# Optimization experiments

Hardware: AMD Instinct MI355X
Metric: run time of the kernel (lower is better)

The kernel has to match this reference:

```python
import jax, jax.numpy as jnp
import numpy as np

B, N, D = 8, 2048, 256
C = 8192  # codebook_size
H = 1     # num_codebooks


def setup_inputs() -> dict:
    key = jax.random.key(0)
    k1, k2 = jax.random.split(key)
    x = jax.random.normal(k1, (B, N, D), dtype=jnp.float32)
    # kaiming_uniform_ on [H, C, D]: bound = sqrt(6 / fan_in), fan_in = C*D for a 3D tensor
    bound = float(np.sqrt(6.0 / (C * D)))
    embed = jax.random.uniform(k2, (H, C, D), dtype=jnp.float32, minval=-bound, maxval=bound)
    return {"x": x, "embed": embed}


def reference(x, embed):
    # x: [B, N, D]; module adds a codebook dim since ndim < 4, flattens to [H, B*N, D]
    flat = x.reshape(1, -1, x.shape[-1]).astype(jnp.float32)  # [H, M, D], M = B*N
    # squared euclidean distance (argmin identical to argmin of cdist p=2)
    x2 = jnp.sum(flat * flat, axis=-1, keepdims=True)              # [H, M, 1]
    e2 = jnp.sum(embed * embed, axis=-1)[:, None, :]               # [H, 1, C]
    xe = jnp.einsum('hmd,hcd->hmc', flat, embed)                   # [H, M, C]
    d2 = x2 - 2.0 * xe + e2                                        # [H, M, C]
    # sample_codebook_temp == 0 -> pure argmax of -dist == argmin of dist
    ind = jnp.argmin(d2, axis=-1)                                  # [H, M]
    quantize = jnp.take(embed[0], ind[0], axis=0).reshape(x.shape) # [B, N, D]
    embed_ind = ind.reshape(x.shape[:-1])                          # [B, N]
    return quantize, embed_ind
```

## Files before the change

kernel.cpp:

```cpp
#include <hip/hip_runtime.h>
#include <hip/hip_bf16.h>

#define M_TOT 16384
#define D_DIM 256
#define C_TOT 8192
#define NCH 4
#define CCH (C_TOT / NCH)
#define QOFF (M_TOT * D_DIM)
#define NPART 8

typedef _Float16 f16;
typedef __attribute__((ext_vector_type(8))) _Float16 f16x8;
typedef __attribute__((ext_vector_type(4))) float f32x4;

#define WS_X2 0
#define WS_E2 (M_TOT)
#define WS_BV (M_TOT + C_TOT)
#define WS_BI (WS_BV + NPART * M_TOT)
#define WS_SPL (WS_BI + NPART * M_TOT)
#define XH_OFF ((size_t)0)
#define XL_OFF ((size_t)M_TOT * D_DIM)
#define EH_OFF ((size_t)2 * M_TOT * D_DIM)
#define EL_OFF ((size_t)2 * M_TOT * D_DIM + (size_t)C_TOT * D_DIM)
#define SPL_HALFS ((size_t)2 * M_TOT * D_DIM + (size_t)2 * C_TOT * D_DIM)
#define WS_NEED ((size_t)WS_SPL * 4 + SPL_HALFS * 2)

__device__ __forceinline__ void gll16(const void* g, void* l) {
    __builtin_amdgcn_global_load_lds((const __attribute__((address_space(1))) void*)g,
                                     (__attribute__((address_space(3))) void*)l, 16, 0, 0);
}

__global__ void split_kernel(const float* __restrict__ x, const float* __restrict__ e,
                             f16* __restrict__ sp, float* __restrict__ x2, float* __restrict__ e2)
{
    int row  = blockIdx.x * 4 + (threadIdx.x >> 6);
    int lane = threadIdx.x & 63;
    bool isx = row < M_TOT;
    int r = isx ? row : row - M_TOT;
    const float* src = (isx ? x : e) + (size_t)r * D_DIM;
    float4 v = *(const float4*)(src + lane * 4);
    float s = v.x * v.x + v.y * v.y + v.z * v.z + v.w * v.w;
    #pragma unroll
    for (int off = 32; off >= 1; off >>= 1) s += __shfl_xor(s, off, 64);
    float sc = isx ? 256.0f : 16384.0f;
    float a[4] = {v.x * sc, v.y * sc, v.z * sc, v.w * sc};
    union { f16 h[4]; ushort4 u; } hh, ll;
    #pragma unroll
    for (int i = 0; i < 4; ++i) {
        f16 h = (f16)a[i];
        hh.h[i] = h;
        ll.h[i] = (f16)(a[i] - (float)h);
    }
    size_t base = (size_t)r * D_DIM + lane * 4;
    f16* ph = sp + (isx ? XH_OFF : EH_OFF) + base;
    f16* pl = sp + (isx ? XL_OFF : EL_OFF) + base;
    *(ushort4*)ph = hh.u;
    *(ushort4*)pl = ll.u;
    if (lane == 0) { if (isx) x2[r] = s; else e2[r] = s; }
}

__global__ __launch_bounds__(512, 2) void mdist_kernel(
    const f16* __restrict__ sp, const float* __restrict__ x2, const float* __restrict__ e2,
    float* __restrict__ bestv, int* __restrict__ besti)
{
    __shared__ __align__(16) f16 lds[65536];

    const int t  = threadIdx.x;
    const int l  = t & 63;
    const int wv = t >> 6;
    const int wr = wv >> 1, wc = wv & 1;
    const int mt = (int)blockIdx.x >> 2;
    const int ch = (int)blockIdx.x & 3;
    const int m0 = mt * 256, c0 = ch * CCH;

    const int q  = l >> 4;
    const int fr = l & 15;

    const int wvh = wv >> 2, rb = wv & 3;
    const f16* gxh = sp + XH_OFF + (size_t)(m0 + rb * 64 + l) * D_DIM;
    const f16* gxl = sp + XL_OFF + (size_t)(m0 + rb * 64 + l) * D_DIM;
    const int bkb = wv & 3;
    const f16* gB = sp + ((wv < 4) ? EH_OFF : EL_OFF)
                    + (size_t)(c0 + (l >> 5) * 128 + (l & 31)) * D_DIM;
    const int btn_b = (wv < 4) ? 32768 : 49152;

    auto STAGE_A = [&](int buf, int ktv) {
        char* lb = (char*)&lds[0] + buf * 65536;
        #pragma unroll
        for (int j = 0; j < 2; ++j) {
            int kb = j * 2 + wvh;
            gll16(gxh + ktv * 32 + kb * 8, lb + 0     + kb * 4096 + rb * 1024 + l * 16);
        }
        #pragma unroll
        for (int j = 0; j < 2; ++j) {
            int kb = j * 2 + wvh;
            gll16(gxl + ktv * 32 + kb * 8, lb + 16384 + kb * 4096 + rb * 1024 + l * 16);
        }
    };
    auto STAGE_B = [&](int buf, int ktv, int ctv, int p) {
        char* lb = (char*)&lds[0] + buf * 65536;
        gll16(gB + (size_t)(ctv * 256 + 32 * p) * D_DIM + ktv * 32 + bkb * 8,
              lb + btn_b + p * 4096 + bkb * 1024 + l * 16);
    };

    float bst[16]; int bix[16];
    #pragma unroll
    for (int i = 0; i < 16; ++i) { bst[i] = 3.4e38f; bix[i] = 0; }

    STAGE_A(0, 0);
    STAGE_B(0, 0, 0, 0);
    STAGE_B(0, 0, 0, 1);
    STAGE_B(0, 0, 0, 2);
    STAGE_B(0, 0, 0, 3);

    for (int ct = 0; ct < 8; ++ct) {
        const int cb = c0 + ct * 256;
        f32x4 acc[4][8];
        #pragma unroll
        for (int m = 0; m < 4; ++m)
            #pragma unroll
            for (int n = 0; n < 8; ++n)
                #pragma unroll
                for (int k = 0; k < 4; ++k) acc[m][n][k] = 0.f;

        #pragma unroll 1
        for (int kt = 0; kt < 8; ++kt) {
            const int cur = (ct * 8 + kt) & 1;
            const f16* L = &lds[0] + cur * 32768;
            const int nbuf = cur ^ 1;
            int nkt = kt + 1, nct = ct;
            if (nkt == 8) { nkt = 0; nct = (ct + 1) & 7; }

            f16x8 ah[4], al[4];

            #pragma unroll
            for (int p = 0; p < 4; ++p) {
                if (p == 0) asm volatile("s_waitcnt vmcnt(3)" ::: "memory");
                else        asm volatile("s_waitcnt vmcnt(7)" ::: "memory");
                __builtin_amdgcn_s_barrier();
                __builtin_amdgcn_sched_barrier(0);

                if (p == 0) STAGE_A(nbuf, nkt);
                STAGE_B(nbuf, nkt, nct, p);

                if (p == 0) {
                    #pragma unroll
                    for (int m = 0; m < 4; ++m) {
                        int aoff = (q * 256 + wr * 64 + m * 16 + fr) * 8;
                        ah[m] = *(const f16x8*)(L + aoff);
                        al[m] = *(const f16x8*)(L + 8192 + aoff);
                    }
                }
                const int bbase = 16384 + p * 2048 + q * 512 + wc * 256;
                f16x8 bh0 = *(const f16x8*)(L + bbase        + (fr)      * 8);
                f16x8 bh1 = *(const f16x8*)(L + bbase        + (16 + fr) * 8);
                f16x8 bl0 = *(const f16x8*)(L + bbase + 8192 + (fr)      * 8);
                f16x8 bl1 = *(const f16x8*)(L + bbase + 8192 + (16 + fr) * 8);
                const int n0 = 2 * p, n1 = 2 * p + 1;

                __builtin_amdgcn_s_setprio(1);
                #pragma unroll
                for (int m = 0; m < 4; ++m)
                    acc[m][n0] = __builtin_amdgcn_mfma_f32_16x16x32_f16(ah[m], bh0, acc[m][n0], 0, 0, 0);
                #pragma unroll
                for (int m = 0; m < 4; ++m)
                    acc[m][n1] = __builtin_amdgcn_mfma_f32_16x16x32_f16(ah[m], bh1, acc[m][n1], 0, 0, 0);
                #pragma unroll
                for (int m = 0; m < 4; ++m)
                    acc[m][n0] = __builtin_amdgcn_mfma_f32_16x16x32_f16(ah[m], bl0, acc[m][n0], 0, 0, 0);
                #pragma unroll
                for (int m = 0; m < 4; ++m)
                    acc[m][n1] = __builtin_amdgcn_mfma_f32_16x16x32_f16(ah[m], bl1, acc[m][n1], 0, 0, 0);
                #pragma unroll
                for (int m = 0; m < 4; ++m)
                    acc[m][n0] = __builtin_amdgcn_mfma_f32_16x16x32_f16(al[m], bh0, acc[m][n0], 0, 0, 0);
                #pragma unroll
                for (int m = 0; m < 4; ++m)
                    acc[m][n1] = __builtin_amdgcn_mfma_f32_16x16x32_f16(al[m], bh1, acc[m][n1], 0, 0, 0);
                __builtin_amdgcn_s_setprio(0);
            }
        }

        float e2v[8];
        #pragma unroll
        for (int n = 0; n < 8; ++n) e2v[n] = e2[cb + wc * 128 + n * 16 + fr];
        #pragma unroll
        for (int m = 0; m < 4; ++m) {
            f32x4 x2v = *(const f32x4*)(x2 + m0 + wr * 64 + m * 16 + q * 4);
            #pragma unroll
            for (int j = 0; j < 4; ++j) {
                const int bi = m * 4 + j;
                #pragma unroll
                for (int n = 0; n < 8; ++n) {
                    float d = fmaf(acc[m][n][j], -0x1p-21f, x2v[j]) + e2v[n];
                    int c = cb + wc * 128 + n * 16 + fr;
                    if (d < bst[bi]) { bst[bi] = d; bix[bi] = c; }
                }
            }
        }
    }

    #pragma unroll
    for (int i = 0; i < 16; ++i) {
        float v = bst[i]; int idx = bix[i];
        #pragma unroll
        for (int off = 8; off >= 1; off >>= 1) {
            float ov = __shfl_xor(v, off, 64);
            int   oi = __shfl_xor(idx, off, 64);
            if (ov < v || (ov == v && oi < idx)) { v = ov; idx = oi; }
        }
        if (fr == 0) {
            int row = m0 + wr * 64 + (i >> 2) * 16 + q * 4 + (i & 3);
            int p = ch * 2 + wc;
            bestv[p * M_TOT + row] = v;
            besti[p * M_TOT + row] = idx;
        }
    }
}

__global__ void finalize_kernel(const float* __restrict__ e,
                                const float* __restrict__ bestv,
                                const int* __restrict__ besti,
                                float* __restrict__ out, int npart)
{
    int m    = blockIdx.x * 4 + (threadIdx.x >> 6);
    int lane = threadIdx.x & 63;
    float bv = bestv[m]; int bi = besti[m];
    for (int h = 1; h < npart; ++h) {
        float v = bestv[h * M_TOT + m];
        int   i2 = besti[h * M_TOT + m];
        if (v < bv || (v == bv && i2 < bi)) { bv = v; bi = i2; }
    }
    if (lane == 0) out[QOFF + m] = (float)bi;
    float4 v = *(const float4*)(e + (size_t)bi * D_DIM + lane * 4);
    *(float4*)(out + (size_t)m * D_DIM + lane * 4) = v;
}

#define BMm 128
#define BNn 128
#define BKk 16
#define BSW 144
#define NKT (D_DIM / BKk)
#define NCT (CCH / BNn)

__device__ __forceinline__ int pcol(int c) { return c + ((c >> 5) << 2); }

__global__ void sq_kernel(const float* __restrict__ x, const float* __restrict__ e,
                          float* __restrict__ x2, float* __restrict__ e2) {
    int row  = blockIdx.x * 4 + (threadIdx.x >> 6);
    int lane = threadIdx.x & 63;
    const float* src = (row < M_TOT) ? (x + (size_t)row * D_DIM)
                                     : (e + (size_t)(row - M_TOT) * D_DIM);
    float4 v = *(const float4*)(src + lane * 4);
    float s = v.x * v.x + v.y * v.y + v.z * v.z + v.w * v.w;
    #pragma unroll
    for (int off = 32; off >= 1; off >>= 1) s += __shfl_xor(s, off, 64);
    if (lane == 0) { if (row < M_TOT) x2[row] = s; else e2[row - M_TOT] = s; }
}

__global__ __launch_bounds__(256, 1) void dist_kernel(
    const float* __restrict__ x, const float* __restrict__ e,
    const float* __restrict__ x2, const float* __restrict__ e2,
    float* __restrict__ bestv, int* __restrict__ besti)
{
    __shared__ __align__(16) float As[2][BKk][BMm];
    __shared__ __align__(16) float Bs[2][BKk][BSW];
    const int t  = threadIdx.x;
    const int ty = t >> 4, tx = t & 15;
    const int mt = (int)blockIdx.x >> 2;
    const int ch = (int)blockIdx.x & 3;
    const int m0 = mt * BMm, c0 = ch * CCH;
    float x2r[8];
    #pragma unroll
    for (int i = 0; i < 8; ++i) x2r[i] = x2[m0 + ty * 8 + i];
    float best[8]; int bidx[8];
    #pragma unroll
    for (int i = 0; i < 8; ++i) { best[i] = 3.4e38f; bidx[i] = 0; }
    const int r0  = t >> 2;
    const int cq0 = (t & 3) << 2;
    for (int ct = 0; ct < NCT; ++ct) {
        const int cb = c0 + ct * BNn;
        float acc[8][8];
        #pragma unroll
        for (int i = 0; i < 8; ++i)
            #pragma unroll
            for (int j = 0; j < 8; ++j) acc[i][j] = 0.f;
        #pragma unroll
        for (int it = 0; it < 2; ++it) {
            int r = r0 + it * 64;
            float4 va = *(const float4*)(x + (size_t)(m0 + r) * D_DIM + cq0);
            float4 vb = *(const float4*)(e + (size_t)(cb + r) * D_DIM + cq0);
            As[0][cq0 + 0][r] = va.x; As[0][cq0 + 1][r] = va.y;
            As[0][cq0 + 2][r] = va.z; As[0][cq0 + 3][r] = va.w;
            int pr = pcol(r);
            Bs[0][cq0 + 0][pr] = vb.x; Bs[0][cq0 + 1][pr] = vb.y;
            Bs[0][cq0 + 2][pr] = vb.z; Bs[0][cq0 + 3][pr] = vb.w;
        }
        __syncthreads();
        #pragma unroll 1
        for (int kt = 0; kt < NKT; ++kt) {
            const int cur = kt & 1;
            float4 pa[2], pb[2];
            if (kt + 1 < NKT) {
                const int k0 = (kt + 1) * BKk;
                #pragma unroll
                for (int it = 0; it < 2; ++it) {
                    int r = r0 + it * 64;
                    pa[it] = *(const float4*)(x + (size_t)(m0 + r) * D_DIM + k0 + cq0);
                    pb[it] = *(const float4*)(e + (size_t)(cb + r) * D_DIM + k0 + cq0);
                }
            }
            #pragma unroll
            for (int k = 0; k < BKk; ++k) {
                float a[8], b[8];
                *(float4*)&a[0] = *(const float4*)&As[cur][k][ty * 8];
                *(float4*)&a[4] = *(const float4*)&As[cur][k][ty * 8 + 4];
                const int pb0 = pcol(tx * 8);
                *(float4*)&b[0] = *(const float4*)&Bs[cur][k][pb0];
                *(float4*)&b[4] = *(const float4*)&Bs[cur][k][pb0 + 4];
                #pragma unroll
                for (int i = 0; i < 8; ++i)
                    #pragma unroll
                    for (int j = 0; j < 8; ++j)
                        acc[i][j] = fmaf(a[i], b[j], acc[i][j]);
            }
            __syncthreads();
            if (kt + 1 < NKT) {
                const int nb = cur ^ 1;
                #pragma unroll
                for (int it = 0; it < 2; ++it) {
                    int r = r0 + it * 64;
                    As[nb][cq0 + 0][r] = pa[it].x; As[nb][cq0 + 1][r] = pa[it].y;
                    As[nb][cq0 + 2][r] = pa[it].z; As[nb][cq0 + 3][r] = pa[it].w;
                    int pr = pcol(r);
                    Bs[nb][cq0 + 0][pr] = pb[it].x; Bs[nb][cq0 + 1][pr] = pb[it].y;
                    Bs[nb][cq0 + 2][pr] = pb[it].z; Bs[nb][cq0 + 3][pr] = pb[it].w;
                }
                __syncthreads();
            }
        }
        float e2v[8];
        #pragma unroll
        for (int j = 0; j < 8; ++j) e2v[j] = e2[cb + tx * 8 + j];
        #pragma unroll
        for (int i = 0; i < 8; ++i) {
            #pragma unroll
            for (int j = 0; j < 8; ++j) {
                float d = (x2r[i] - 2.0f * acc[i][j]) + e2v[j];
                int c = cb + tx * 8 + j;
                if (d < best[i]) { best[i] = d; bidx[i] = c; }
            }
        }
    }
    #pragma unroll
    for (int i = 0; i < 8; ++i) {
        float v = best[i]; int idx = bidx[i];
        #pragma unroll
        for (int off = 8; off >= 1; off >>= 1) {
            float ov = __shfl_xor(v, off, 64);
            int   oi = __shfl_xor(idx, off, 64);
            if (ov < v || (ov == v && oi < idx)) { v = ov; idx = oi; }
        }
        if (tx == 0) {
            int row = m0 + ty * 8 + i;
            bestv[ch * M_TOT + row] = v;
            besti[ch * M_TOT + row] = idx;
        }
    }
}

extern "C" void kernel_launch(void* const* d_in, const int* in_sizes, int n_in,
                              void* d_out, int out_size, void* d_ws, size_t ws_size,
                              hipStream_t stream) {
    const float* x = (const float*)d_in[0];
    const float* e = (const float*)d_in[1];
    float* out = (float*)d_out;

    float* wsf   = (float*)d_ws;
    float* x2    = wsf + WS_X2;
    float* e2    = wsf + WS_E2;
    float* bestv = wsf + WS_BV;
    int*   besti = (int*)(wsf + WS_BI);

    if (ws_size >= WS_NEED) {
        f16* sp = (f16*)(wsf + WS_SPL);
        split_kernel<<<(M_TOT + C_TOT) / 4, 256, 0, stream>>>(x, e, sp, x2, e2);
        mdist_kernel<<<(M_TOT / 256) * NCH, 512, 0, stream>>>(sp, x2, e2, bestv, besti);
        finalize_kernel<<<M_TOT / 4, 256, 0, stream>>>(e, bestv, besti, out, NPART);
    } else {
        sq_kernel<<<(M_TOT + C_TOT) / 4, 256, 0, stream>>>(x, e, x2, e2);
        dist_kernel<<<(M_TOT / BMm) * NCH, 256, 0, stream>>>(x, e, x2, e2, bestv, besti);
        finalize_kernel<<<M_TOT / 4, 256, 0, stream>>>(e, bestv, besti, out, NCH);
    }
}
```

Measured before the change: 224.9 us.

## Switch distance GEMM to 32x32x16 MFMA with per-tile shuffle argmin reduction

Replaces the 16x16x32 f16 MFMA tiling with 32x32x16 MFMA, rearranging the A/B LDS fragment reads and the accumulator layout to match. The argmin epilogue now reduces each codebook tile across lanes right away with shuffles, so each lane keeps a single running best instead of 16. The aim is fewer MFMA issues and fewer LDS fragment loads per tile, plus lower register pressure. In exchange, shuffle-reduction work moves into every codebook tile instead of happening once at the end.

```diff
diff --git a/kernel.cpp b/kernel.cpp
--- a/kernel.cpp
+++ b/kernel.cpp
@@ -12,6 +12,7 @@
 typedef _Float16 f16;
 typedef __attribute__((ext_vector_type(8))) _Float16 f16x8;
 typedef __attribute__((ext_vector_type(4))) float f32x4;
+typedef __attribute__((ext_vector_type(16))) float f32x16;
 
 #define WS_X2 0
 #define WS_E2 (M_TOT)
@@ -73,9 +74,6 @@
     const int ch = (int)blockIdx.x & 3;
     const int m0 = mt * 256, c0 = ch * CCH;
 
-    const int q  = l >> 4;
-    const int fr = l & 15;
-
     const int wvh = wv >> 2, rb = wv & 3;
     const f16* gxh = sp + XH_OFF + (size_t)(m0 + rb * 64 + l) * D_DIM;
     const f16* gxl = sp + XL_OFF + (size_t)(m0 + rb * 64 + l) * D_DIM;
@@ -103,9 +101,9 @@
               lb + btn_b + p * 4096 + bkb * 1024 + l * 16);
     };
 
-    float bst[16]; int bix[16];
-    #pragma unroll
-    for (int i = 0; i < 16; ++i) { bst[i] = 3.4e38f; bix[i] = 0; }
+    float bst = 3.4e38f; int bix = 0;
+    const int myl = l & 31;
+    const int hf  = l >> 5;
 
     STAGE_A(0, 0);
     STAGE_B(0, 0, 0, 0);
@@ -115,13 +113,13 @@
 
     for (int ct = 0; ct < 8; ++ct) {
         const int cb = c0 + ct * 256;
-        f32x4 acc[4][8];
-        #pragma unroll
-        for (int m = 0; m < 4; ++m)
-            #pragma unroll
-            for (int n = 0; n < 8; ++n)
-                #pragma unroll
-                for (int k = 0; k < 4; ++k) acc[m][n][k] = 0.f;
+        f32x16 acc[2][4];
+        #pragma unroll
+        for (int mm = 0; mm < 2; ++mm)
+            #pragma unroll
+            for (int nn = 0; nn < 4; ++nn)
+                #pragma unroll
+                for (int k = 0; k < 16; ++k) acc[mm][nn][k] = 0.f;
 
         #pragma unroll 1
         for (int kt = 0; kt < 8; ++kt) {
@@ -131,7 +129,7 @@
             int nkt = kt + 1, nct = ct;
             if (nkt == 8) { nkt = 0; nct = (ct + 1) & 7; }
 
-            f16x8 ah[4], al[4];
+            f16x8 ah[2][2], al[2][2];
 
             #pragma unroll
             for (int p = 0; p < 4; ++p) {
@@ -145,76 +143,75 @@
 
                 if (p == 0) {
                     #pragma unroll
-                    for (int m = 0; m < 4; ++m) {
-                        int aoff = (q * 256 + wr * 64 + m * 16 + fr) * 8;
-                        ah[m] = *(const f16x8*)(L + aoff);
-                        al[m] = *(const f16x8*)(L + 8192 + aoff);
-                    }
-                }
-                const int bbase = 16384 + p * 2048 + q * 512 + wc * 256;
-                f16x8 bh0 = *(const f16x8*)(L + bbase        + (fr)      * 8);
-                f16x8 bh1 = *(const f16x8*)(L + bbase        + (16 + fr) * 8);
-                f16x8 bl0 = *(const f16x8*)(L + bbase + 8192 + (fr)      * 8);
-                f16x8 bl1 = *(const f16x8*)(L + bbase + 8192 + (16 + fr) * 8);
-                const int n0 = 2 * p, n1 = 2 * p + 1;
+                    for (int mm = 0; mm < 2; ++mm)
+                        #pragma unroll
+                        for (int s = 0; s < 2; ++s) {
+                            int aoff = (2 * s + hf) * 2048 + (wr * 64 + mm * 32 + myl) * 8;
+                            ah[mm][s] = *(const f16x8*)(L + aoff);
+                            al[mm][s] = *(const f16x8*)(L + 8192 + aoff);
+                        }
+                }
+                const int bb  = 16384 + p * 2048 + wc * 256 + myl * 8;
+                const int kbo = hf * 512;
+                f16x8 bh_s0 = *(const f16x8*)(L + bb + kbo);
+                f16x8 bh_s1 = *(const f16x8*)(L + bb + 1024 + kbo);
+                f16x8 bl_s0 = *(const f16x8*)(L + bb + 8192 + kbo);
+                f16x8 bl_s1 = *(const f16x8*)(L + bb + 8192 + 1024 + kbo);
 
                 __builtin_amdgcn_s_setprio(1);
                 #pragma unroll
-                for (int m = 0; m < 4; ++m)
-                    acc[m][n0] = __builtin_amdgcn_mfma_f32_16x16x32_f16(ah[m], bh0, acc[m][n0], 0, 0, 0);
-                #pragma unroll
-                for (int m = 0; m < 4; ++m)
-                    acc[m][n1] = __builtin_amdgcn_mfma_f32_16x16x32_f16(ah[m], bh1, acc[m][n1], 0, 0, 0);
-                #pragma unroll
-                for (int m = 0; m < 4; ++m)
-                    acc[m][n0] = __builtin_amdgcn_mfma_f32_16x16x32_f16(ah[m], bl0, acc[m][n0], 0, 0, 0);
-                #pragma unroll
-                for (int m = 0; m < 4; ++m)
-                    acc[m][n1] = __builtin_amdgcn_mfma_f32_16x16x32_f16(ah[m], bl1, acc[m][n1], 0, 0, 0);
-                #pragma unroll
-                for (int m = 0; m < 4; ++m)
-                    acc[m][n0] = __builtin_amdgcn_mfma_f32_16x16x32_f16(al[m], bh0, acc[m][n0], 0, 0, 0);
-                #pragma unroll
-                for (int m = 0; m < 4; ++m)
-                    acc[m][n1] = __builtin_amdgcn_mfma_f32_16x16x32_f16(al[m], bh1, acc[m][n1], 0, 0, 0);
+                for (int s = 0; s < 2; ++s) {
+                    f16x8 BH = (s == 0) ? bh_s0 : bh_s1;
+                    f16x8 BL = (s == 0) ? bl_s0 : bl_s1;
+                    acc[0][p] = __builtin_amdgcn_mfma_f32_32x32x16_f16(ah[0][s], BH, acc[0][p], 0, 0, 0);
+                    acc[1][p] = __builtin_amdgcn_mfma_f32_32x32x16_f16(ah[1][s], BH, acc[1][p], 0, 0, 0);
+                    acc[0][p] = __builtin_amdgcn_mfma_f32_32x32x16_f16(ah[0][s], BL, acc[0][p], 0, 0, 0);
+                    acc[1][p] = __builtin_amdgcn_mfma_f32_32x32x16_f16(ah[1][s], BL, acc[1][p], 0, 0, 0);
+                    acc[0][p] = __builtin_amdgcn_mfma_f32_32x32x16_f16(al[0][s], BH, acc[0][p], 0, 0, 0);
+                    acc[1][p] = __builtin_amdgcn_mfma_f32_32x32x16_f16(al[1][s], BH, acc[1][p], 0, 0, 0);
+                }
                 __builtin_amdgcn_s_setprio(0);
             }
         }
 
-        float e2v[8];
-        #pragma unroll
-        for (int n = 0; n < 8; ++n) e2v[n] = e2[cb + wc * 128 + n * 16 + fr];
-        #pragma unroll
-        for (int m = 0; m < 4; ++m) {
-            f32x4 x2v = *(const f32x4*)(x2 + m0 + wr * 64 + m * 16 + q * 4);
-            #pragma unroll
-            for (int j = 0; j < 4; ++j) {
-                const int bi = m * 4 + j;
-                #pragma unroll
-                for (int n = 0; n < 8; ++n) {
-                    float d = fmaf(acc[m][n][j], -0x1p-21f, x2v[j]) + e2v[n];
-                    int c = cb + wc * 128 + n * 16 + fr;
-                    if (d < bst[bi]) { bst[bi] = d; bix[bi] = c; }
-                }
-            }
-        }
-    }
-
-    #pragma unroll
-    for (int i = 0; i < 16; ++i) {
-        float v = bst[i]; int idx = bix[i];
-        #pragma unroll
-        for (int off = 8; off >= 1; off >>= 1) {
-            float ov = __shfl_xor(v, off, 64);
-            int   oi = __shfl_xor(idx, off, 64);
-            if (ov < v || (ov == v && oi < idx)) { v = ov; idx = oi; }
-        }
-        if (fr == 0) {
-            int row = m0 + wr * 64 + (i >> 2) * 16 + q * 4 + (i & 3);
-            int p = ch * 2 + wc;
-            bestv[p * M_TOT + row] = v;
-            besti[p * M_TOT + row] = idx;
-        }
+        float e2v[4];
+        #pragma unroll
+        for (int nn = 0; nn < 4; ++nn) e2v[nn] = e2[cb + wc * 128 + nn * 32 + myl];
+        #pragma unroll
+        for (int mm = 0; mm < 2; ++mm) {
+            const int rbase = m0 + wr * 64 + mm * 32 + 4 * hf;
+            f32x4 x2q[4];
+            #pragma unroll
+            for (int j = 0; j < 4; ++j) x2q[j] = *(const f32x4*)(x2 + rbase + 8 * j);
+            #pragma unroll
+            for (int reg = 0; reg < 16; ++reg) {
+                const float xv = x2q[reg >> 2][reg & 3];
+                float v = fmaf(acc[mm][0][reg], -0x1p-21f, xv) + e2v[0];
+                int  ci = cb + wc * 128 + myl;
+                #pragma unroll
+                for (int nn = 1; nn < 4; ++nn) {
+                    float d = fmaf(acc[mm][nn][reg], -0x1p-21f, xv) + e2v[nn];
+                    if (d < v) { v = d; ci = cb + wc * 128 + nn * 32 + myl; }
+                }
+                #pragma unroll
+                for (int off = 16; off >= 1; off >>= 1) {
+                    float ov = __shfl_xor(v, off, 64);
+                    int   oi = __shfl_xor(ci, off, 64);
+                    if (ov < v || (ov == v && oi < ci)) { v = ov; ci = oi; }
+                }
+                if (myl == mm * 16 + reg) {
+                    if (v < bst) { bst = v; bix = ci; }
+                }
+            }
+        }
+    }
+
+    {
+        const int mm = myl >> 4, rg = myl & 15;
+        int row = m0 + wr * 64 + mm * 32 + (rg & 3) + 8 * (rg >> 2) + 4 * hf;
+        int p = ch * 2 + wc;
+        bestv[p * M_TOT + row] = bst;
+        besti[p * M_TOT + row] = bix;
     }
 }
 
@@ -241,7 +238,7 @@
 #define BKk 16
 #define BSW 144
 #define NKT (D_DIM / BKk)
-#define NCT (CCH / BNn)
+#define NCTF (CCH / BNn)
 
 __device__ __forceinline__ int pcol(int c) { return c + ((c >> 5) << 2); }
 
@@ -278,7 +275,7 @@
     for (int i = 0; i < 8; ++i) { best[i] = 3.4e38f; bidx[i] = 0; }
     const int r0  = t >> 2;
     const int cq0 = (t & 3) << 2;
-    for (int ct = 0; ct < NCT; ++ct) {
+    for (int ct = 0; ct < NCTF; ++ct) {
         const int cb = c0 + ct * BNn;
         float acc[8][8];
         #pragma unroll
```

Result: slower. 332.6 us (+47.8%).
